# Performance work log

Measured on AMD Instinct MI355X. Metric: run time of the kernel, lower is better.

## Reference

```python
import math
import jax, jax.numpy as jnp
import numpy as np

B, S, H, NH = 8, 1024, 1024, 16
HD = H // NH  # head dim = 64

def setup_inputs() -> dict:
    key = jax.random.key(0)
    ks = jax.random.split(key, 4)
    scale = 1.0 / math.sqrt(H)
    return {
        "hidden_state": jax.random.normal(ks[0], (B, S, H), jnp.float32),
        "attention_mask": jnp.ones((B, 1, S), jnp.float32),
        "Wq": jax.random.normal(ks[1], (H, H), jnp.float32) * scale,
        "bq": jnp.zeros((H,), jnp.float32),
        "Wk": jax.random.normal(ks[2], (H, H), jnp.float32) * scale,
        "bk": jnp.zeros((H,), jnp.float32),
        "Wv": jax.random.normal(ks[3], (H, H), jnp.float32) * scale,
        "bv": jnp.zeros((H,), jnp.float32),
    }

def _split_heads(x):
    # [B,S,H] -> [B,NH,S,HD]
    return x.reshape(B, S, NH, HD).transpose(0, 2, 1, 3)

def reference(hidden_state, attention_mask, Wq, bq, Wk, bk, Wv, bv):
    q = _split_heads(hidden_state @ Wq.T + bq)
    k = _split_heads(hidden_state @ Wk.T + bk)
    v = _split_heads(hidden_state @ Wv.T + bv)
    scores = jnp.einsum("bhqd,bhkd->bhqk", q, k) / math.sqrt(HD)
    # mask [B,1,S] -> additive bias [B,1,S,1], broadcast over heads and keys
    bias = (1.0 - attention_mask)[..., None] * -10000.0
    scores = scores + bias
    probs = jax.nn.softmax(scores, axis=-1)  # dropout prob = 0.0 (eval)
    ctx = jnp.einsum("bhqk,bhkd->bhqd", probs, v)
    return ctx.transpose(0, 2, 1, 3).reshape(B, S, H)
```

## Files before the change

kernel.cpp:

```cpp
#include <hip/hip_runtime.h>
#include <hip/hip_bf16.h>


typedef __attribute__((ext_vector_type(8))) short bf16x8;
typedef __attribute__((ext_vector_type(4))) float f32x4;
typedef unsigned short u16;

#define NB 8
#define NS 1024
#define NH_ 16
#define HD_ 64
#define QKV_T (NB * NH_ * NS * HD_)
#define XN (8192 * 1024)
#define WN (1024 * 1024)
#define QSCL 0.180336880f

static __device__ __forceinline__ u16 f2bf(float f) {
    unsigned int u = __float_as_uint(f);
    u += 0x7FFFu + ((u >> 16) & 1u);
    return (u16)(u >> 16);
}

static __device__ __forceinline__ bf16x8 cvt8(const float* p) {
    float4 a = *(const float4*)p;
    float4 b = *(const float4*)(p + 4);
    union { bf16x8 v; u16 s[8]; } r;
    r.s[0] = f2bf(a.x); r.s[1] = f2bf(a.y); r.s[2] = f2bf(a.z); r.s[3] = f2bf(a.w);
    r.s[4] = f2bf(b.x); r.s[5] = f2bf(b.y); r.s[6] = f2bf(b.z); r.s[7] = f2bf(b.w);
    return r.v;
}

static __device__ __forceinline__ void async16(const u16* g, u16* l) {
    __builtin_amdgcn_global_load_lds((const __attribute__((address_space(1))) void*)g,
                                     (__attribute__((address_space(3))) void*)l,
                                     16, 0, 0);
}

__global__ __launch_bounds__(256) void cvt_pass(
    const float* __restrict__ X,
    const float* __restrict__ Wq, const float* __restrict__ Wk,
    const float* __restrict__ Wv,
    u16* __restrict__ Xb, u16* __restrict__ Wb)
{
    size_t i8 = ((size_t)blockIdx.x * 256 + threadIdx.x) * 8;
    if (i8 < XN) {
        *(bf16x8*)(Xb + i8) = cvt8(X + i8);
    } else {
        size_t j = i8 - XN;
        int w = (int)(j >> 20);
        const float* src = (w == 0) ? Wq : (w == 1) ? Wk : Wv;
        *(bf16x8*)(Wb + j) = cvt8(src + (j & (WN - 1)));
    }
}

__global__ __launch_bounds__(256) void qkv_gemm_bf16(
    const u16* __restrict__ Xb, const u16* __restrict__ Wb,
    const float* __restrict__ bq, const float* __restrict__ bk,
    const float* __restrict__ bv,
    u16* __restrict__ qkv)
{
    __shared__ u16 As[128 * 64];
    __shared__ u16 Bs[128 * 64];

    const int tid  = threadIdx.x;
    const int lane = tid & 63;
    const int wid  = tid >> 6;
    const int l15  = lane & 15;
    const int quad = lane >> 4;
    const int sw   = l15 & 7;
    const int wm   = (wid >> 1) * 64;
    const int wn   = (wid & 1) * 64;

    const int bid = blockIdx.x;
    const int x   = bid & 7;
    const int j   = bid >> 3;
    const int m0  = (x * 8 + (j & 7)) * 128;
    const int nb  = (j >> 3) * 128;

    f32x4 acc[4][4];
#pragma unroll
    for (int mi = 0; mi < 4; ++mi)
#pragma unroll
        for (int ni = 0; ni < 4; ++ni) acc[mi][ni] = (f32x4){0.f, 0.f, 0.f, 0.f};

    for (int kt = 0; kt < 16; ++kt) {
#pragma unroll
        for (int it = 0; it < 4; ++it) {
            int idx = it * 256 + tid;
            int row = idx >> 3, kc = idx & 7;
            int kcs = (kc ^ (row & 7)) * 8;
            async16(Xb + (size_t)(m0 + row) * 1024 + kt * 64 + kcs, As + idx * 8);
            async16(Wb + (size_t)(nb + row) * 1024 + kt * 64 + kcs, Bs + idx * 8);
        }
        __syncthreads();
#pragma unroll
        for (int kk = 0; kk < 2; ++kk) {
            bf16x8 a[4], b[4];
#pragma unroll
            for (int mi = 0; mi < 4; ++mi)
                a[mi] = *(const bf16x8*)&As[(wm + mi * 16 + l15) * 64 + (((kk * 4 + quad) ^ sw) * 8)];
#pragma unroll
            for (int ni = 0; ni < 4; ++ni)
                b[ni] = *(const bf16x8*)&Bs[(wn + ni * 16 + l15) * 64 + (((kk * 4 + quad) ^ sw) * 8)];
#pragma unroll
            for (int mi = 0; mi < 4; ++mi)
#pragma unroll
                for (int ni = 0; ni < 4; ++ni)
                    acc[mi][ni] = __builtin_amdgcn_mfma_f32_16x16x32_bf16(
                        a[mi], b[ni], acc[mi][ni], 0, 0, 0);
        }
        __syncthreads();
    }

    const int which = nb >> 10;
    const int ncol0 = nb & 1023;
    const int batch = m0 >> 10;
    const float* bias = (which == 0) ? bq : (which == 1) ? bk : bv;
    const float scl   = (which == 0) ? QSCL : 1.0f;
#pragma unroll
    for (int ni = 0; ni < 4; ++ni) {
        int nn = ncol0 + wn + ni * 16 + l15;
        float bia = bias[nn];
        int h = nn >> 6;
        int d = nn & 63;
        size_t base = (size_t)((which * NB + batch) * NH_ + h) * (NS * HD_);
        if (which == 2) {
#pragma unroll
            for (int mi = 0; mi < 4; ++mi) {
                int s_base = ((m0 + wm + mi * 16 + quad * 4) & 1023);
                ushort4 pk;
                pk.x = f2bf(acc[mi][ni][0] + bia);
                pk.y = f2bf(acc[mi][ni][1] + bia);
                pk.z = f2bf(acc[mi][ni][2] + bia);
                pk.w = f2bf(acc[mi][ni][3] + bia);
                *(ushort4*)&qkv[base + (size_t)d * NS + s_base] = pk;
            }
        } else {
#pragma unroll
            for (int mi = 0; mi < 4; ++mi) {
#pragma unroll
                for (int r = 0; r < 4; ++r) {
                    int s = (m0 + wm + mi * 16 + quad * 4 + r) & 1023;
                    qkv[base + (size_t)s * HD_ + d] = f2bf((acc[mi][ni][r] + bia) * scl);
                }
            }
        }
    }
}

__global__ __launch_bounds__(256) void qkv_gemm_f32(
    const float* __restrict__ X,
    const float* __restrict__ Wq, const float* __restrict__ bq,
    const float* __restrict__ Wk, const float* __restrict__ bk,
    const float* __restrict__ Wv, const float* __restrict__ bv,
    u16* __restrict__ qkv)
{
    __shared__ u16 As[128 * 72];
    __shared__ u16 Bs[128 * 72];
    const int tid  = threadIdx.x;
    const int lane = tid & 63;
    const int wid  = tid >> 6;
    const int l15  = lane & 15;
    const int quad = lane >> 4;
    const int wm   = (wid >> 1) * 64;
    const int wn   = (wid & 1) * 64;
    const int m0   = blockIdx.x * 128;
    const int nb   = blockIdx.y * 128;
    const int which = nb >> 10;
    const int ncol0 = nb & 1023;
    const float* W    = (which == 0) ? Wq : (which == 1) ? Wk : Wv;
    const float* bias = (which == 0) ? bq : (which == 1) ? bk : bv;
    const float scl   = (which == 0) ? QSCL : 1.0f;

    f32x4 acc[4][4];
#pragma unroll
    for (int mi = 0; mi < 4; ++mi)
#pragma unroll
        for (int ni = 0; ni < 4; ++ni) acc[mi][ni] = (f32x4){0.f, 0.f, 0.f, 0.f};

    for (int kt = 0; kt < 16; ++kt) {
#pragma unroll
        for (int it = 0; it < 4; ++it) {
            int idx = it * 256 + tid;
            int row = idx >> 3, c = idx & 7;
            *(bf16x8*)&As[row * 72 + c * 8] = cvt8(&X[(size_t)(m0 + row) * 1024 + kt * 64 + c * 8]);
            *(bf16x8*)&Bs[row * 72 + c * 8] = cvt8(&W[(size_t)(ncol0 + row) * 1024 + kt * 64 + c * 8]);
        }
        __syncthreads();
#pragma unroll
        for (int kk = 0; kk < 2; ++kk) {
            bf16x8 a[4], b[4];
#pragma unroll
            for (int mi = 0; mi < 4; ++mi)
                a[mi] = *(const bf16x8*)&As[(wm + mi * 16 + l15) * 72 + kk * 32 + quad * 8];
#pragma unroll
            for (int ni = 0; ni < 4; ++ni)
                b[ni] = *(const bf16x8*)&Bs[(wn + ni * 16 + l15) * 72 + kk * 32 + quad * 8];
#pragma unroll
            for (int mi = 0; mi < 4; ++mi)
#pragma unroll
                for (int ni = 0; ni < 4; ++ni)
                    acc[mi][ni] = __builtin_amdgcn_mfma_f32_16x16x32_bf16(
                        a[mi], b[ni], acc[mi][ni], 0, 0, 0);
        }
        __syncthreads();
    }
#pragma unroll
    for (int ni = 0; ni < 4; ++ni) {
        int nn = ncol0 + wn + ni * 16 + l15;
        float bia = bias[nn];
        int h = nn >> 6;
        int d = nn & 63;
#pragma unroll
        for (int mi = 0; mi < 4; ++mi) {
#pragma unroll
            for (int r = 0; r < 4; ++r) {
                int rg    = m0 + wm + mi * 16 + quad * 4 + r;
                int batch = rg >> 10;
                int s     = rg & 1023;
                size_t base = (size_t)((which * NB + batch) * NH_ + h) * (NS * HD_);
                size_t off  = (which == 2) ? base + (size_t)d * NS + s
                                           : base + (size_t)s * HD_ + d;
                qkv[off] = f2bf((acc[mi][ni][r] + bia) * scl);
            }
        }
    }
}

__global__ __launch_bounds__(256) void attn(
    const u16* __restrict__ qkv, float* __restrict__ out)
{
    __shared__ u16 Qs[128 * 64];
    __shared__ u16 Ks[2][64 * 64];
    __shared__ u16 VTs[2][64 * 64];
    __shared__ u16 Ps[128 * 72];

    const int tid  = threadIdx.x;
    const int lane = tid & 63;
    const int wid  = tid >> 6;
    const int l15  = lane & 15;
    const int quad = lane >> 4;
    const int sw   = l15 & 7;
    const int q0   = blockIdx.x * 128;
    const int h    = blockIdx.y;
    const int batch = blockIdx.z;

    const size_t headoff = (size_t)(batch * NH_ + h) * (NS * HD_);
    const u16* Qg = qkv + headoff;
    const u16* Kg = qkv + (size_t)QKV_T + headoff;
    const u16* Vt = qkv + (size_t)2 * QKV_T + headoff;

    const u16* kp[2];
    const u16* vp[2];
#pragma unroll
    for (int it = 0; it < 2; ++it) {
        int idx = it * 256 + tid;
        int row = idx >> 3, kc = idx & 7;
        int kcs = (kc ^ (row & 7)) * 8;
        kp[it] = Kg + (size_t)row * 64 + kcs;
        vp[it] = Vt + (size_t)row * NS + kcs;
    }

#pragma unroll
    for (int it = 0; it < 4; ++it) {
        int idx = it * 256 + tid;
        int row = idx >> 3, kc = idx & 7;
        int kcs = (kc ^ (row & 7)) * 8;
        async16(Qg + (size_t)(q0 + row) * 64 + kcs, Qs + idx * 8);
    }
#pragma unroll
    for (int it = 0; it < 2; ++it) {
        int idx = it * 256 + tid;
        async16(kp[it], Ks[0] + idx * 8);
        async16(vp[it], VTs[0] + idx * 8);
    }
    __syncthreads();

    bf16x8 aq[2][2];
#pragma unroll
    for (int f = 0; f < 2; ++f) {
        aq[f][0] = *(const bf16x8*)&Qs[(wid * 32 + f * 16 + l15) * 64 + ((quad ^ sw) * 8)];
        aq[f][1] = *(const bf16x8*)&Qs[(wid * 32 + f * 16 + l15) * 64 + (((4 + quad) ^ sw) * 8)];
    }

    float lsum[2][4] = {{0.f, 0.f, 0.f, 0.f}, {0.f, 0.f, 0.f, 0.f}};
    f32x4 o[2][4];
#pragma unroll
    for (int f = 0; f < 2; ++f)
#pragma unroll
        for (int ni = 0; ni < 4; ++ni) o[f][ni] = (f32x4){0.f, 0.f, 0.f, 0.f};

    for (int kt = 0; kt < 16; ++kt) {
        const u16* Kc = Ks[kt & 1];
        const u16* Vc = VTs[kt & 1];

        if (kt < 15) {
            u16* Kn = Ks[(kt & 1) ^ 1];
            u16* Vn = VTs[(kt & 1) ^ 1];
#pragma unroll
            for (int it = 0; it < 2; ++it) {
                int idx = it * 256 + tid;
                async16(kp[it] + (size_t)(kt + 1) * 4096, Kn + idx * 8);
                async16(vp[it] + (size_t)(kt + 1) * 64, Vn + idx * 8);
            }
        }

        f32x4 sfr[2][4];
#pragma unroll
        for (int ni = 0; ni < 4; ++ni) {
            bf16x8 b0 = *(const bf16x8*)&Kc[(ni * 16 + l15) * 64 + ((quad ^ sw) * 8)];
            bf16x8 b1 = *(const bf16x8*)&Kc[(ni * 16 + l15) * 64 + (((4 + quad) ^ sw) * 8)];
#pragma unroll
            for (int f = 0; f < 2; ++f) {
                f32x4 sa = (f32x4){0.f, 0.f, 0.f, 0.f};
                sa = __builtin_amdgcn_mfma_f32_16x16x32_bf16(aq[f][0], b0, sa, 0, 0, 0);
                sa = __builtin_amdgcn_mfma_f32_16x16x32_bf16(aq[f][1], b1, sa, 0, 0, 0);
                sfr[f][ni] = sa;
            }
        }

#pragma unroll
        for (int f = 0; f < 2; ++f)
#pragma unroll
            for (int ni = 0; ni < 4; ++ni)
#pragma unroll
                for (int r = 0; r < 4; ++r) {
                    float p = __builtin_amdgcn_exp2f(sfr[f][ni][r]);
                    lsum[f][r] += p;
                    Ps[(wid * 32 + f * 16 + quad * 4 + r) * 72 + ni * 16 + l15] = f2bf(p);
                }

#pragma unroll
        for (int kk = 0; kk < 2; ++kk) {
            bf16x8 ap[2];
#pragma unroll
            for (int f = 0; f < 2; ++f)
                ap[f] = *(const bf16x8*)&Ps[(wid * 32 + f * 16 + l15) * 72 + kk * 32 + quad * 8];
#pragma unroll
            for (int ni = 0; ni < 4; ++ni) {
                bf16x8 bv_ = *(const bf16x8*)&Vc[(ni * 16 + l15) * 64 + (((kk * 4 + quad) ^ sw) * 8)];
#pragma unroll
                for (int f = 0; f < 2; ++f)
                    o[f][ni] = __builtin_amdgcn_mfma_f32_16x16x32_bf16(ap[f], bv_, o[f][ni], 0, 0, 0);
            }
        }
        __syncthreads();
    }

#pragma unroll
    for (int f = 0; f < 2; ++f)
#pragma unroll
        for (int r = 0; r < 4; ++r)
#pragma unroll
            for (int msk = 1; msk <= 8; msk <<= 1)
                lsum[f][r] += __shfl_xor(lsum[f][r], msk, 64);

#pragma unroll
    for (int f = 0; f < 2; ++f)
#pragma unroll
        for (int ni = 0; ni < 4; ++ni)
#pragma unroll
            for (int r = 0; r < 4; ++r) {
                int row = wid * 32 + f * 16 + quad * 4 + r;
                out[(size_t)(batch * NS + q0 + row) * 1024 + h * 64 + ni * 16 + l15] =
                    o[f][ni][r] / lsum[f][r];
            }
}

extern "C" void kernel_launch(void* const* d_in, const int* in_sizes, int n_in,
                              void* d_out, int out_size, void* d_ws, size_t ws_size,
                              hipStream_t stream) {
    const float* X  = (const float*)d_in[0];
    const float* Wq = (const float*)d_in[2];
    const float* bq = (const float*)d_in[3];
    const float* Wk = (const float*)d_in[4];
    const float* bk = (const float*)d_in[5];
    const float* Wv = (const float*)d_in[6];
    const float* bv = (const float*)d_in[7];
    float* outp = (float*)d_out;

    u16* qkv = (u16*)d_ws;
    u16* Xb  = (u16*)((char*)d_ws + (size_t)QKV_T * 3 * 2);
    u16* Wb  = Xb + XN;
    const size_t need = (size_t)QKV_T * 3 * 2 + (size_t)XN * 2 + (size_t)3 * WN * 2;

    if (ws_size >= need) {
        cvt_pass<<<(XN + 3 * WN) / 8 / 256, 256, 0, stream>>>(X, Wq, Wk, Wv, Xb, Wb);
        qkv_gemm_bf16<<<1536, 256, 0, stream>>>(Xb, Wb, bq, bk, bv, qkv);
    } else {
        qkv_gemm_f32<<<dim3(64, 24), 256, 0, stream>>>(X, Wq, bq, Wk, bk, Wv, bv, qkv);
    }
    attn<<<dim3(8, 16, 8), 256, 0, stream>>>(qkv, outp);
}
```

Before: 236.7 us.

## Restructure attention to single-wave blocks loading K/V directly into registers

The attention kernel now runs one 64-thread wave per 32-query block and loads K and V fragments straight from global memory into registers instead of staging shared tiles in LDS. K fragments for the next tile are prefetched into a second register set, the P tile uses an XOR-swizzled small LDS buffer, and probabilities are converted with a packed bf16 conversion. This removes block-wide barriers and most LDS traffic and allows more resident blocks. In exchange, K/V reuse across waves is lost, so global/L2 traffic rises and register pressure grows.

```diff
diff --git a/kernel.cpp b/kernel.cpp
--- a/kernel.cpp
+++ b/kernel.cpp
@@ -19,6 +19,17 @@
     unsigned int u = __float_as_uint(f);
     u += 0x7FFFu + ((u >> 16) & 1u);
     return (u16)(u >> 16);
+}
+
+static __device__ __forceinline__ unsigned int pk2bf(float a, float b) {
+#if __has_builtin(__builtin_amdgcn_cvt_pk_bf16_f32)
+    typedef __attribute__((ext_vector_type(2))) __bf16 bf16x2_t;
+    union { bf16x2_t v; unsigned int u; } c;
+    c.v = __builtin_amdgcn_cvt_pk_bf16_f32(a, b);
+    return c.u;
+#else
+    return (unsigned int)f2bf(a) | ((unsigned int)f2bf(b) << 16);
+#endif
 }
 
 static __device__ __forceinline__ bf16x8 cvt8(const float* p) {
@@ -227,21 +238,15 @@
     }
 }
 
-__global__ __launch_bounds__(256) void attn(
+__global__ __launch_bounds__(64, 2) void attn(
     const u16* __restrict__ qkv, float* __restrict__ out)
 {
-    __shared__ u16 Qs[128 * 64];
-    __shared__ u16 Ks[2][64 * 64];
-    __shared__ u16 VTs[2][64 * 64];
-    __shared__ u16 Ps[128 * 72];
-
-    const int tid  = threadIdx.x;
-    const int lane = tid & 63;
-    const int wid  = tid >> 6;
+    __shared__ u16 Ps[32 * 72];
+
+    const int lane = threadIdx.x & 63;
     const int l15  = lane & 15;
     const int quad = lane >> 4;
-    const int sw   = l15 & 7;
-    const int q0   = blockIdx.x * 128;
+    const int q0   = blockIdx.x * 32;
     const int h    = blockIdx.y;
     const int batch = blockIdx.z;
 
@@ -250,38 +255,22 @@
     const u16* Kg = qkv + (size_t)QKV_T + headoff;
     const u16* Vt = qkv + (size_t)2 * QKV_T + headoff;
 
-    const u16* kp[2];
-    const u16* vp[2];
-#pragma unroll
-    for (int it = 0; it < 2; ++it) {
-        int idx = it * 256 + tid;
-        int row = idx >> 3, kc = idx & 7;
-        int kcs = (kc ^ (row & 7)) * 8;
-        kp[it] = Kg + (size_t)row * 64 + kcs;
-        vp[it] = Vt + (size_t)row * NS + kcs;
-    }
-
-#pragma unroll
-    for (int it = 0; it < 4; ++it) {
-        int idx = it * 256 + tid;
-        int row = idx >> 3, kc = idx & 7;
-        int kcs = (kc ^ (row & 7)) * 8;
-        async16(Qg + (size_t)(q0 + row) * 64 + kcs, Qs + idx * 8);
-    }
-#pragma unroll
-    for (int it = 0; it < 2; ++it) {
-        int idx = it * 256 + tid;
-        async16(kp[it], Ks[0] + idx * 8);
-        async16(vp[it], VTs[0] + idx * 8);
-    }
-    __syncthreads();
-
     bf16x8 aq[2][2];
 #pragma unroll
-    for (int f = 0; f < 2; ++f) {
-        aq[f][0] = *(const bf16x8*)&Qs[(wid * 32 + f * 16 + l15) * 64 + ((quad ^ sw) * 8)];
-        aq[f][1] = *(const bf16x8*)&Qs[(wid * 32 + f * 16 + l15) * 64 + (((4 + quad) ^ sw) * 8)];
-    }
+    for (int f = 0; f < 2; ++f)
+#pragma unroll
+        for (int kk = 0; kk < 2; ++kk)
+            aq[f][kk] = *(const bf16x8*)&Qg[(size_t)(q0 + f * 16 + l15) * 64 + kk * 32 + quad * 8];
+
+    const u16* kbase = Kg + (size_t)l15 * 64 + quad * 8;
+    const u16* vbase = Vt + (size_t)l15 * 1024 + quad * 8;
+
+    bf16x8 bk[4][2], bk2[4][2], bv[4][2];
+#pragma unroll
+    for (int ni = 0; ni < 4; ++ni)
+#pragma unroll
+        for (int kk = 0; kk < 2; ++kk)
+            bk[ni][kk] = *(const bf16x8*)&kbase[ni * 1024 + kk * 32];
 
     float lsum[2][4] = {{0.f, 0.f, 0.f, 0.f}, {0.f, 0.f, 0.f, 0.f}};
     f32x4 o[2][4];
@@ -290,61 +279,75 @@
 #pragma unroll
         for (int ni = 0; ni < 4; ++ni) o[f][ni] = (f32x4){0.f, 0.f, 0.f, 0.f};
 
+    const int wr_c8base = (l15 >> 3);
+    const int rd_key    = (l15 >> 2) & 3;
+
     for (int kt = 0; kt < 16; ++kt) {
-        const u16* Kc = Ks[kt & 1];
-        const u16* Vc = VTs[kt & 1];
-
-        if (kt < 15) {
-            u16* Kn = Ks[(kt & 1) ^ 1];
-            u16* Vn = VTs[(kt & 1) ^ 1];
-#pragma unroll
-            for (int it = 0; it < 2; ++it) {
-                int idx = it * 256 + tid;
-                async16(kp[it] + (size_t)(kt + 1) * 4096, Kn + idx * 8);
-                async16(vp[it] + (size_t)(kt + 1) * 64, Vn + idx * 8);
-            }
-        }
+#pragma unroll
+        for (int ni = 0; ni < 4; ++ni)
+#pragma unroll
+            for (int kk = 0; kk < 2; ++kk)
+                bv[ni][kk] = *(const bf16x8*)&vbase[ni * 16384 + kt * 64 + kk * 32];
 
         f32x4 sfr[2][4];
 #pragma unroll
-        for (int ni = 0; ni < 4; ++ni) {
-            bf16x8 b0 = *(const bf16x8*)&Kc[(ni * 16 + l15) * 64 + ((quad ^ sw) * 8)];
-            bf16x8 b1 = *(const bf16x8*)&Kc[(ni * 16 + l15) * 64 + (((4 + quad) ^ sw) * 8)];
+        for (int ni = 0; ni < 4; ++ni)
 #pragma unroll
             for (int f = 0; f < 2; ++f) {
                 f32x4 sa = (f32x4){0.f, 0.f, 0.f, 0.f};
-                sa = __builtin_amdgcn_mfma_f32_16x16x32_bf16(aq[f][0], b0, sa, 0, 0, 0);
-                sa = __builtin_amdgcn_mfma_f32_16x16x32_bf16(aq[f][1], b1, sa, 0, 0, 0);
+                sa = __builtin_amdgcn_mfma_f32_16x16x32_bf16(aq[f][0], bk[ni][0], sa, 0, 0, 0);
+                sa = __builtin_amdgcn_mfma_f32_16x16x32_bf16(aq[f][1], bk[ni][1], sa, 0, 0, 0);
                 sfr[f][ni] = sa;
             }
+
+        if (kt < 15) {
+#pragma unroll
+            for (int ni = 0; ni < 4; ++ni)
+#pragma unroll
+                for (int kk = 0; kk < 2; ++kk)
+                    bk2[ni][kk] = *(const bf16x8*)&kbase[(kt + 1) * 4096 + ni * 1024 + kk * 32];
         }
 
 #pragma unroll
         for (int f = 0; f < 2; ++f)
 #pragma unroll
-            for (int ni = 0; ni < 4; ++ni)
-#pragma unroll
-                for (int r = 0; r < 4; ++r) {
-                    float p = __builtin_amdgcn_exp2f(sfr[f][ni][r]);
-                    lsum[f][r] += p;
-                    Ps[(wid * 32 + f * 16 + quad * 4 + r) * 72 + ni * 16 + l15] = f2bf(p);
-                }
+            for (int ni = 0; ni < 4; ++ni) {
+                float p0 = __builtin_amdgcn_exp2f(sfr[f][ni][0]);
+                float p1 = __builtin_amdgcn_exp2f(sfr[f][ni][1]);
+                float p2 = __builtin_amdgcn_exp2f(sfr[f][ni][2]);
+                float p3 = __builtin_amdgcn_exp2f(sfr[f][ni][3]);
+                lsum[f][0] += p0; lsum[f][1] += p1;
+                lsum[f][2] += p2; lsum[f][3] += p3;
+                unsigned int w01 = pk2bf(p0, p1);
+                unsigned int w23 = pk2bf(p2, p3);
+                int c8 = ((ni * 2 + wr_c8base) ^ quad) * 8 + (l15 & 7);
+                u16* p = &Ps[(f * 16 + quad * 4) * 72 + c8];
+                p[0]       = (u16)w01;
+                p[72]      = (u16)(w01 >> 16);
+                p[144]     = (u16)w23;
+                p[216]     = (u16)(w23 >> 16);
+            }
 
 #pragma unroll
         for (int kk = 0; kk < 2; ++kk) {
             bf16x8 ap[2];
 #pragma unroll
             for (int f = 0; f < 2; ++f)
-                ap[f] = *(const bf16x8*)&Ps[(wid * 32 + f * 16 + l15) * 72 + kk * 32 + quad * 8];
-#pragma unroll
-            for (int ni = 0; ni < 4; ++ni) {
-                bf16x8 bv_ = *(const bf16x8*)&Vc[(ni * 16 + l15) * 64 + (((kk * 4 + quad) ^ sw) * 8)];
+                ap[f] = *(const bf16x8*)&Ps[(f * 16 + l15) * 72 + (((kk * 4 + quad) ^ rd_key) * 8)];
+#pragma unroll
+            for (int ni = 0; ni < 4; ++ni)
 #pragma unroll
                 for (int f = 0; f < 2; ++f)
-                    o[f][ni] = __builtin_amdgcn_mfma_f32_16x16x32_bf16(ap[f], bv_, o[f][ni], 0, 0, 0);
-            }
-        }
-        __syncthreads();
+                    o[f][ni] = __builtin_amdgcn_mfma_f32_16x16x32_bf16(ap[f], bv[ni][kk], o[f][ni], 0, 0, 0);
+        }
+
+        if (kt < 15) {
+#pragma unroll
+            for (int ni = 0; ni < 4; ++ni)
+#pragma unroll
+                for (int kk = 0; kk < 2; ++kk)
+                    bk[ni][kk] = bk2[ni][kk];
+        }
     }
 
 #pragma unroll
@@ -361,7 +364,7 @@
         for (int ni = 0; ni < 4; ++ni)
 #pragma unroll
             for (int r = 0; r < 4; ++r) {
-                int row = wid * 32 + f * 16 + quad * 4 + r;
+                int row = f * 16 + quad * 4 + r;
                 out[(size_t)(batch * NS + q0 + row) * 1024 + h * 64 + ni * 16 + l15] =
                     o[f][ni][r] / lsum[f][r];
             }
@@ -390,5 +393,5 @@
     } else {
         qkv_gemm_f32<<<dim3(64, 24), 256, 0, stream>>>(X, Wq, bq, Wk, bk, Wv, bv, qkv);
     }
-    attn<<<dim3(8, 16, 8), 256, 0, stream>>>(qkv, outp);
-}
+    attn<<<dim3(32, 16, 8), 64, 0, stream>>>(qkv, outp);
+}
```

New measurement: 293.1 us. +23.8%, slower.

## Stage Q/K GEMM epilogue through LDS for vectorized stores; load Q directly to registers

Applied to the files above, without the earlier changes.

The bf16 QKV GEMM epilogue for Q and K now writes the tile into dynamic shared memory (row stride 132) and then issues coalesced 16-byte stores into the head-major layout. Previously each thread wrote scattered 2-byte stores. The attention kernel drops its Q shared-memory staging and loads Q fragments straight from global memory into registers. This frees LDS and removes one sync dependency. In exchange, the GEMM uses more dynamic LDS (about 33 KB) and adds an extra barrier, and the direct Q global loads are uncoalesced per lane.

```diff
diff --git a/kernel.cpp b/kernel.cpp
--- a/kernel.cpp
+++ b/kernel.cpp
@@ -53,14 +53,17 @@
     }
 }
 
+#define GEMM_LDS_BYTES (128 * 132 * 2)
 __global__ __launch_bounds__(256) void qkv_gemm_bf16(
     const u16* __restrict__ Xb, const u16* __restrict__ Wb,
     const float* __restrict__ bq, const float* __restrict__ bk,
     const float* __restrict__ bv,
     u16* __restrict__ qkv)
 {
-    __shared__ u16 As[128 * 64];
-    __shared__ u16 Bs[128 * 64];
+    extern __shared__ u16 smem[];
+    u16* As = smem;
+    u16* Bs = smem + 128 * 64;
+    u16* Cs = smem;
 
     const int tid  = threadIdx.x;
     const int lane = tid & 63;
@@ -117,14 +120,15 @@
     const int batch = m0 >> 10;
     const float* bias = (which == 0) ? bq : (which == 1) ? bk : bv;
     const float scl   = (which == 0) ? QSCL : 1.0f;
-#pragma unroll
-    for (int ni = 0; ni < 4; ++ni) {
-        int nn = ncol0 + wn + ni * 16 + l15;
-        float bia = bias[nn];
-        int h = nn >> 6;
-        int d = nn & 63;
-        size_t base = (size_t)((which * NB + batch) * NH_ + h) * (NS * HD_);
-        if (which == 2) {
+
+    if (which == 2) {
+#pragma unroll
+        for (int ni = 0; ni < 4; ++ni) {
+            int nn = ncol0 + wn + ni * 16 + l15;
+            float bia = bias[nn];
+            int h = nn >> 6;
+            int d = nn & 63;
+            size_t base = (size_t)((2 * NB + batch) * NH_ + h) * (NS * HD_);
 #pragma unroll
             for (int mi = 0; mi < 4; ++mi) {
                 int s_base = ((m0 + wm + mi * 16 + quad * 4) & 1023);
@@ -135,15 +139,31 @@
                 pk.w = f2bf(acc[mi][ni][3] + bia);
                 *(ushort4*)&qkv[base + (size_t)d * NS + s_base] = pk;
             }
-        } else {
-#pragma unroll
-            for (int mi = 0; mi < 4; ++mi) {
-#pragma unroll
-                for (int r = 0; r < 4; ++r) {
-                    int s = (m0 + wm + mi * 16 + quad * 4 + r) & 1023;
-                    qkv[base + (size_t)s * HD_ + d] = f2bf((acc[mi][ni][r] + bia) * scl);
-                }
-            }
+        }
+    } else {
+#pragma unroll
+        for (int ni = 0; ni < 4; ++ni) {
+            int col = wn + ni * 16 + l15;
+            float bia = bias[ncol0 + col];
+#pragma unroll
+            for (int mi = 0; mi < 4; ++mi)
+#pragma unroll
+                for (int r = 0; r < 4; ++r)
+                    Cs[(wm + mi * 16 + quad * 4 + r) * 132 + col] =
+                        f2bf((acc[mi][ni][r] + bia) * scl);
+        }
+        __syncthreads();
+        const size_t tb = (size_t)((which * NB + batch) * NH_) * (NS * HD_);
+        const int h0 = ncol0 >> 6;
+#pragma unroll
+        for (int it = 0; it < 8; ++it) {
+            int idx = it * 256 + tid;
+            int row = idx >> 4;
+            int c   = idx & 15;
+            int h   = h0 + (c >> 3);
+            int s   = (m0 + row) & 1023;
+            *(uint4*)&qkv[tb + (size_t)h * (NS * HD_) + (size_t)s * HD_ + (c & 7) * 8] =
+                *(const uint4*)&Cs[row * 132 + c * 8];
         }
     }
 }
@@ -230,7 +250,6 @@
 __global__ __launch_bounds__(256) void attn(
     const u16* __restrict__ qkv, float* __restrict__ out)
 {
-    __shared__ u16 Qs[128 * 64];
     __shared__ u16 Ks[2][64 * 64];
     __shared__ u16 VTs[2][64 * 64];
     __shared__ u16 Ps[128 * 72];
@@ -261,13 +280,13 @@
         vp[it] = Vt + (size_t)row * NS + kcs;
     }
 
-#pragma unroll
-    for (int it = 0; it < 4; ++it) {
-        int idx = it * 256 + tid;
-        int row = idx >> 3, kc = idx & 7;
-        int kcs = (kc ^ (row & 7)) * 8;
-        async16(Qg + (size_t)(q0 + row) * 64 + kcs, Qs + idx * 8);
-    }
+    bf16x8 aq[2][2];
+#pragma unroll
+    for (int f = 0; f < 2; ++f)
+#pragma unroll
+        for (int kk = 0; kk < 2; ++kk)
+            aq[f][kk] = *(const bf16x8*)&Qg[(size_t)(q0 + wid * 32 + f * 16 + l15) * 64 + kk * 32 + quad * 8];
+
 #pragma unroll
     for (int it = 0; it < 2; ++it) {
         int idx = it * 256 + tid;
@@ -275,13 +294,6 @@
         async16(vp[it], VTs[0] + idx * 8);
     }
     __syncthreads();
-
-    bf16x8 aq[2][2];
-#pragma unroll
-    for (int f = 0; f < 2; ++f) {
-        aq[f][0] = *(const bf16x8*)&Qs[(wid * 32 + f * 16 + l15) * 64 + ((quad ^ sw) * 8)];
-        aq[f][1] = *(const bf16x8*)&Qs[(wid * 32 + f * 16 + l15) * 64 + (((4 + quad) ^ sw) * 8)];
-    }
 
     float lsum[2][4] = {{0.f, 0.f, 0.f, 0.f}, {0.f, 0.f, 0.f, 0.f}};
     f32x4 o[2][4];
@@ -386,7 +398,7 @@
 
     if (ws_size >= need) {
         cvt_pass<<<(XN + 3 * WN) / 8 / 256, 256, 0, stream>>>(X, Wq, Wk, Wv, Xb, Wb);
-        qkv_gemm_bf16<<<1536, 256, 0, stream>>>(Xb, Wb, bq, bk, bv, qkv);
+        qkv_gemm_bf16<<<1536, 256, GEMM_LDS_BYTES, stream>>>(Xb, Wb, bq, bk, bv, qkv);
     } else {
         qkv_gemm_f32<<<dim3(64, 24), 256, 0, stream>>>(X, Wq, bq, Wk, bk, Wv, bv, qkv);
     }
```

Result: faster. 231.8 us (-2.1%).
